# Kernel optimization log

Measured on AMD Instinct MI355X. Metric: run time of the kernel, lower is better.

## Reference

```python
import jax, jax.numpy as jnp
import numpy as np
from jax.ops import segment_sum

NEG_SLOPE = 0.01  # torch F.leaky_relu default

N_NODES = 100000
N_EDGES = 1600000
IN_FEAT = 67
HIDDEN = 256
N_CLASS = 18
N_GRAPHS = 256


def setup_inputs() -> dict:
    key = jax.random.key(0)
    ks = jax.random.split(key, 12)
    h = jax.random.normal(ks[0], (N_NODES, IN_FEAT), dtype=jnp.float32)
    src = jax.random.randint(ks[1], (N_EDGES,), 0, N_NODES, dtype=jnp.int32)
    dst = jax.random.randint(ks[2], (N_EDGES,), 0, N_NODES, dtype=jnp.int32)
    graph_ids = jnp.sort(jax.random.randint(ks[3], (N_NODES,), 0, N_GRAPHS, dtype=jnp.int32))
    s = 0.05
    W1_self = jax.random.normal(ks[4], (IN_FEAT, HIDDEN), dtype=jnp.float32) * s
    W1_neigh = jax.random.normal(ks[5], (IN_FEAT, HIDDEN), dtype=jnp.float32) * s
    b1 = jnp.zeros((HIDDEN,), dtype=jnp.float32)
    W2_self = jax.random.normal(ks[6], (HIDDEN, HIDDEN), dtype=jnp.float32) * s
    W2_neigh = jax.random.normal(ks[7], (HIDDEN, HIDDEN), dtype=jnp.float32) * s
    b2 = jnp.zeros((HIDDEN,), dtype=jnp.float32)
    Wfc = jax.random.normal(ks[8], (HIDDEN, N_CLASS), dtype=jnp.float32) * s
    bfc = jnp.zeros((N_CLASS,), dtype=jnp.float32)
    return {
        "h": h, "W1_self": W1_self, "W1_neigh": W1_neigh, "b1": b1,
        "W2_self": W2_self, "W2_neigh": W2_neigh, "b2": b2,
        "Wfc": Wfc, "bfc": bfc,
        "src": src, "dst": dst, "graph_ids": graph_ids, "num_graphs": N_GRAPHS,
    }


def _sage_mean(h, Wself, Wneigh, b, src, dst, n_nodes):
    # DGL SAGEConv(mean): h_neigh = mean over incoming neighbors; 0 if no neighbors
    agg = segment_sum(h[src], dst, num_segments=n_nodes)          # [N, D]
    deg = segment_sum(jnp.ones_like(dst, dtype=h.dtype), dst, num_segments=n_nodes)
    h_neigh = agg / jnp.maximum(deg, 1.0)[:, None]
    return h @ Wself + h_neigh @ Wneigh + b


def reference(h, W1_self, W1_neigh, b1, W2_self, W2_neigh, b2, Wfc, bfc,
              src, dst, graph_ids, num_graphs):
    n_nodes = h.shape[0]
    x = jax.nn.leaky_relu(_sage_mean(h, W1_self, W1_neigh, b1, src, dst, n_nodes), NEG_SLOPE)
    x = jax.nn.leaky_relu(_sage_mean(x, W2_self, W2_neigh, b2, src, dst, n_nodes), NEG_SLOPE)
    # dgl.mean_nodes: per-graph mean pooling over nodes
    gsum = segment_sum(x, graph_ids, num_segments=num_graphs)       # [G, D]
    gcnt = segment_sum(jnp.ones((n_nodes,), dtype=x.dtype), graph_ids, num_segments=num_graphs)
    hg = gsum / jnp.maximum(gcnt, 1.0)[:, None]
    return hg @ Wfc + bfc  # [G, n_classifier]
```

## Files before the change

kernel.cpp:

```cpp
#include <hip/hip_runtime.h>

#define WAVE 64
#define OW 256
#define LDA1 96
#define NCHUNK 64
#define PBITS 15
#define PBINS (1 << PBITS)
#define NPART 4

typedef short bf16x8 __attribute__((ext_vector_type(8)));
typedef float f32x4  __attribute__((ext_vector_type(4)));
typedef float f32x2  __attribute__((ext_vector_type(2)));

__device__ __forceinline__ unsigned short f2bf(float f) {
    unsigned int u = __float_as_uint(f);
    u = (u + 0x7FFF + ((u >> 16) & 1)) >> 16;
    return (unsigned short)u;
}
__device__ __forceinline__ float bf2f(unsigned short u) {
    return __uint_as_float(((unsigned int)u) << 16);
}
__device__ __forceinline__ float bflo(unsigned int u) { return __uint_as_float(u << 16); }
__device__ __forceinline__ float bfhi(unsigned int u) { return __uint_as_float(u & 0xFFFF0000u); }
__device__ __forceinline__ unsigned int packbf(float lo, float hi) {
    return (unsigned int)f2bf(lo) | ((unsigned int)f2bf(hi) << 16);
}
__device__ __forceinline__ float lrelu(float x) { return x > 0.0f ? x : 0.01f * x; }

__device__ __forceinline__ unsigned int pack4_f8(float v0, float v1, float v2, float v3) {
    int p = __builtin_amdgcn_cvt_pk_fp8_f32(v0, v1, 0, false);
    p = __builtin_amdgcn_cvt_pk_fp8_f32(v2, v3, p, true);
    return (unsigned int)p;
}
__device__ __forceinline__ unsigned char enc1_f8(float v) {
    return (unsigned char)(__builtin_amdgcn_cvt_pk_fp8_f32(v, 0.0f, 0, false) & 0xFF);
}
__device__ __forceinline__ void acc4_f8(float* a, unsigned int u) {
    f32x2 lo = __builtin_amdgcn_cvt_pk_f32_fp8(u, false);
    f32x2 hi = __builtin_amdgcn_cvt_pk_f32_fp8(u, true);
    a[0] += lo.x; a[1] += lo.y; a[2] += hi.x; a[3] += hi.y;
}


__device__ __forceinline__ void pack_b_body(const float* __restrict__ Ws,
                                            const float* __restrict__ Wn,
                                            unsigned short* __restrict__ Bb,
                                            int KHALF, int KT_HALF, int idx) {
    int e  = idx & 7;
    int l  = (idx >> 3) & 63;
    int nt = (idx >> 9) & 15;
    int kt = idx >> 13;
    int n  = nt * 16 + (l & 15);
    int kh = (kt < KT_HALF ? kt : kt - KT_HALF) * 32 + (l >> 4) * 8 + e;
    const float* W = (kt < KT_HALF) ? Ws : Wn;
    float v = (kh < KHALF) ? W[(size_t)kh * OW + n] : 0.0f;
    Bb[idx] = f2bf(v);
}

__global__ void prep_kernel(const float* __restrict__ h, unsigned int* __restrict__ hb,
                            unsigned int* __restrict__ hb8, int N, int K,
                            const float* __restrict__ W1s, const float* __restrict__ W1n,
                            unsigned short* __restrict__ Bb1,
                            const float* __restrict__ W2s, const float* __restrict__ W2n,
                            unsigned short* __restrict__ Bb2) {
    const int tid = blockIdx.x * blockDim.x + threadIdx.x;
    const int nth = gridDim.x * blockDim.x;

    const int tot_h = N * (LDA1 / 2);
    for (int i = tid; i < tot_h; i += nth) {
        int row = i / (LDA1 / 2);
        int c   = (i - row * (LDA1 / 2)) * 2;
        float v0 = (c     < K) ? h[(size_t)row * K + c]     : 0.0f;
        float v1 = (c + 1 < K) ? h[(size_t)row * K + c + 1] : 0.0f;
        hb[i] = packbf(v0, v1);
    }
    const int tot8 = N * (LDA1 / 4);
    for (int i = tid; i < tot8; i += nth) {
        int row = i / (LDA1 / 4);
        int c   = (i - row * (LDA1 / 4)) * 4;
        const float* hr = h + (size_t)row * K;
        float v0 = (c     < K) ? hr[c]     : 0.0f;
        float v1 = (c + 1 < K) ? hr[c + 1] : 0.0f;
        float v2 = (c + 2 < K) ? hr[c + 2] : 0.0f;
        float v3 = (c + 3 < K) ? hr[c + 3] : 0.0f;
        hb8[i] = pack4_f8(v0, v1, v2, v3);
    }
    for (int i = tid; i < 2 * 3 * 16 * 64 * 8; i += nth)
        pack_b_body(W1s, W1n, Bb1, K, 3, i);
    for (int i = tid; i < 2 * 8 * 16 * 64 * 8; i += nth)
        pack_b_body(W2s, W2n, Bb2, OW, 8, i);
}


__global__ __launch_bounds__(512) void hist_kernel(const int* __restrict__ dst, int E, int N,
                                                   unsigned short* __restrict__ hist,
                                                   unsigned short* __restrict__ rank_local) {
    __shared__ unsigned int lcnt[PBINS / 2];
    const int c    = blockIdx.x / NPART;
    const int p    = blockIdx.x - c * NPART;
    const int base = p << PBITS;
    const int nb   = (N - base < PBINS) ? (N - base) : PBINS;
    if (nb <= 0) return;
    const int che = (E + NCHUNK - 1) / NCHUNK;
    const int beg = c * che;
    const int end = (beg + che < E) ? (beg + che) : E;

    for (int i = threadIdx.x; i < PBINS / 2; i += 512) lcnt[i] = 0;
    __syncthreads();

    auto proc = [&](int d, int e) {
        d -= base;
        if ((unsigned)d < (unsigned)nb) {
            unsigned int sh  = (d & 1) * 16;
            unsigned int old = atomicAdd(&lcnt[d >> 1], 1u << sh);
            rank_local[e] = (unsigned short)((old >> sh) & 0xFFFFu);
        }
    };

    if (((beg | end) & 3) == 0) {
        const int4* dst4 = (const int4*)(dst + beg);
        const int n4 = (end - beg) >> 2;
        for (int i = threadIdx.x; i < n4; i += 512) {
            int4 d = dst4[i];
            int e = beg + 4 * i;
            proc(d.x, e + 0);
            proc(d.y, e + 1);
            proc(d.z, e + 2);
            proc(d.w, e + 3);
        }
    } else {
        for (int e = beg + (int)threadIdx.x; e < end; e += 512)
            proc(dst[e], e);
    }
    __syncthreads();

    unsigned short* hrow = hist + (size_t)c * N + base;
    for (int i = threadIdx.x; i < nb; i += 512) {
        unsigned int v = lcnt[i >> 1];
        hrow[i] = (unsigned short)((v >> ((i & 1) * 16)) & 0xFFFFu);
    }
}

__global__ void chunk_scan_kernel(unsigned short* __restrict__ hist, int* __restrict__ cnt,
                                  int N) {
    int bin = blockIdx.x * blockDim.x + threadIdx.x;
    if (bin >= N) return;
    int s = 0;
#pragma unroll 8
    for (int c = 0; c < NCHUNK; ++c) {
        size_t idx = (size_t)c * N + bin;
        int t = hist[idx];
        hist[idx] = (unsigned short)s;
        s += t;
    }
    cnt[bin] = s;
}

__global__ __launch_bounds__(1024) void scan_blocksum(const int* __restrict__ cnt,
                                                      int* __restrict__ bsum, int n) {
    __shared__ int s[1024];
    int i = blockIdx.x * 1024 + threadIdx.x;
    s[threadIdx.x] = (i < n) ? cnt[i] : 0;
    __syncthreads();
    for (int off = 512; off > 0; off >>= 1) {
        if (threadIdx.x < off) s[threadIdx.x] += s[threadIdx.x + off];
        __syncthreads();
    }
    if (threadIdx.x == 0) bsum[blockIdx.x] = s[0];
}

__global__ __launch_bounds__(128) void scan_offsets(int* __restrict__ bsum, int nb) {
    __shared__ int s[128];
    int v = (threadIdx.x < nb) ? bsum[threadIdx.x] : 0;
    s[threadIdx.x] = v;
    __syncthreads();
    for (int off = 1; off < 128; off <<= 1) {
        int t = (threadIdx.x >= off) ? s[threadIdx.x - off] : 0;
        __syncthreads();
        s[threadIdx.x] += t;
        __syncthreads();
    }
    if (threadIdx.x < nb) bsum[threadIdx.x] = s[threadIdx.x] - v;
}

__global__ __launch_bounds__(1024) void scan_write(const int* __restrict__ cnt,
                                                   const int* __restrict__ boff,
                                                   int* __restrict__ rowptr, int n) {
    __shared__ int s[1024];
    int i = blockIdx.x * 1024 + threadIdx.x;
    int v = (i < n) ? cnt[i] : 0;
    s[threadIdx.x] = v;
    __syncthreads();
    for (int off = 1; off < 1024; off <<= 1) {
        int t = (threadIdx.x >= off) ? s[threadIdx.x - off] : 0;
        __syncthreads();
        s[threadIdx.x] += t;
        __syncthreads();
    }
    if (i < n) rowptr[i + 1] = boff[blockIdx.x] + s[threadIdx.x];
    if (i == 0) rowptr[0] = 0;
}

__global__ void fill_kernel(const int* __restrict__ src, const int* __restrict__ dst,
                            const unsigned short* __restrict__ rank_local,
                            const int* __restrict__ rowptr,
                            const unsigned short* __restrict__ hist,
                            int* __restrict__ csr, int E, int N) {
    const int che = (E + NCHUNK - 1) / NCHUNK;
    const int tid = blockIdx.x * blockDim.x + threadIdx.x;
    const int nth = gridDim.x * blockDim.x;

    if ((che & 3) == 0) {
        const int e4 = E >> 2;
        const int4* dst4 = (const int4*)dst;
        const int4* src4 = (const int4*)src;
        const ushort4* r4 = (const ushort4*)rank_local;
        for (int i = tid; i < e4; i += nth) {
            int4 d = dst4[i];
            int4 s = src4[i];
            ushort4 r = r4[i];
            const unsigned short* hrow = hist + (size_t)(4 * i / che) * N;
            csr[rowptr[d.x] + (int)hrow[d.x] + (int)r.x] = s.x;
            csr[rowptr[d.y] + (int)hrow[d.y] + (int)r.y] = s.y;
            csr[rowptr[d.z] + (int)hrow[d.z] + (int)r.z] = s.z;
            csr[rowptr[d.w] + (int)hrow[d.w] + (int)r.w] = s.w;
        }
        for (int e = e4 * 4 + tid; e < E; e += nth) {
            int d = dst[e];
            csr[rowptr[d] + (int)hist[(size_t)(e / che) * N + d] + (int)rank_local[e]] = src[e];
        }
    } else {
        for (int e = tid; e < E; e += nth) {
            int d = dst[e];
            csr[rowptr[d] + (int)hist[(size_t)(e / che) * N + d] + (int)rank_local[e]] = src[e];
        }
    }
}


__global__ void gather_mean256_f8(const unsigned char* __restrict__ feat,
                                  const int* __restrict__ rowptr, const int* __restrict__ csr,
                                  unsigned int* __restrict__ aggm, int N) {
    const int lane = threadIdx.x & (WAVE - 1);
    const int grp  = lane >> 4;
    const int sub  = lane & 15;
    int wave = (blockIdx.x * blockDim.x + threadIdx.x) / WAVE;
    int nw   = (gridDim.x * blockDim.x) / WAVE;

    for (int v = wave; v < N; v += nw) {
        const int beg = rowptr[v], deg = rowptr[v + 1] - beg;
        float a[16];
#pragma unroll
        for (int i = 0; i < 16; ++i) a[i] = 0.0f;

        const int noct = deg >> 3;
        for (int i = 0; i < noct; ++i) {
            int e0 = csr[beg + 8 * i + grp];
            int e1 = csr[beg + 8 * i + 4 + grp];
            uint4 x0 = *(const uint4*)(feat + (size_t)e0 * 256 + sub * 16);
            uint4 x1 = *(const uint4*)(feat + (size_t)e1 * 256 + sub * 16);
            acc4_f8(a + 0,  x0.x); acc4_f8(a + 4,  x0.y);
            acc4_f8(a + 8,  x0.z); acc4_f8(a + 12, x0.w);
            acc4_f8(a + 0,  x1.x); acc4_f8(a + 4,  x1.y);
            acc4_f8(a + 8,  x1.z); acc4_f8(a + 12, x1.w);
        }
        for (int e = (noct << 3) + grp; e < deg; e += 4) {
            int s = csr[beg + e];
            uint4 x = *(const uint4*)(feat + (size_t)s * 256 + sub * 16);
            acc4_f8(a + 0,  x.x); acc4_f8(a + 4,  x.y);
            acc4_f8(a + 8,  x.z); acc4_f8(a + 12, x.w);
        }
#pragma unroll
        for (int i = 0; i < 16; ++i) {
            a[i] += __shfl_xor(a[i], 16);
            a[i] += __shfl_xor(a[i], 32);
        }
        if (grp == 0) {
            float inv = 1.0f / fmaxf((float)deg, 1.0f);
            unsigned int o[8];
#pragma unroll
            for (int i = 0; i < 8; ++i)
                o[i] = packbf(a[2 * i] * inv, a[2 * i + 1] * inv);
            unsigned int* dst0 = aggm + (size_t)v * 128 + sub * 8;
            *(uint4*)(dst0)     = make_uint4(o[0], o[1], o[2], o[3]);
            *(uint4*)(dst0 + 4) = make_uint4(o[4], o[5], o[6], o[7]);
        }
    }
}

__global__ void gather_mean_pad_f8(const unsigned char* __restrict__ feat,
                                   const int* __restrict__ rowptr, const int* __restrict__ csr,
                                   unsigned int* __restrict__ aggm, int N) {
    const int lane = threadIdx.x & (WAVE - 1);
    const int half = lane >> 5;
    const int sub  = lane & 31;
    const bool act = sub < 24;
    int wave = (blockIdx.x * blockDim.x + threadIdx.x) / WAVE;
    int nw   = (gridDim.x * blockDim.x) / WAVE;

    for (int v = wave; v < N; v += nw) {
        const int beg = rowptr[v], deg = rowptr[v + 1] - beg;
        const int npairs = deg >> 1;
        float a[4] = {0.f, 0.f, 0.f, 0.f};

        int p = 0;
        for (; p + 3 < npairs; p += 4) {
            int i0 = csr[beg + 2 * (p + 0) + half];
            int i1 = csr[beg + 2 * (p + 1) + half];
            int i2 = csr[beg + 2 * (p + 2) + half];
            int i3 = csr[beg + 2 * (p + 3) + half];
            if (act) {
                unsigned int x0 = *(const unsigned int*)(feat + (size_t)i0 * 96 + sub * 4);
                unsigned int x1 = *(const unsigned int*)(feat + (size_t)i1 * 96 + sub * 4);
                unsigned int x2 = *(const unsigned int*)(feat + (size_t)i2 * 96 + sub * 4);
                unsigned int x3 = *(const unsigned int*)(feat + (size_t)i3 * 96 + sub * 4);
                acc4_f8(a, x0); acc4_f8(a, x1); acc4_f8(a, x2); acc4_f8(a, x3);
            }
        }
        for (; p < npairs; ++p) {
            int i0 = csr[beg + 2 * p + half];
            if (act) {
                unsigned int x0 = *(const unsigned int*)(feat + (size_t)i0 * 96 + sub * 4);
                acc4_f8(a, x0);
            }
        }
        if ((deg & 1) && half == 0) {
            int i0 = csr[beg + deg - 1];
            if (act) {
                unsigned int x0 = *(const unsigned int*)(feat + (size_t)i0 * 96 + sub * 4);
                acc4_f8(a, x0);
            }
        }
#pragma unroll
        for (int i = 0; i < 4; ++i) a[i] += __shfl_xor(a[i], 32);

        if (half == 0 && act) {
            float inv = 1.0f / fmaxf((float)deg, 1.0f);
            uint2 o;
            o.x = packbf(a[0] * inv, a[1] * inv);
            o.y = packbf(a[2] * inv, a[3] * inv);
            *(uint2*)(aggm + (size_t)v * 48 + sub * 2) = o;
        }
    }
}

template<int KT_HALF, int CHUNK, bool F8OUT>
__global__ __launch_bounds__(256) void sage_mfma(
    const unsigned short* __restrict__ Hs, const unsigned short* __restrict__ Hn, int lda,
    const unsigned short* __restrict__ Bb, const float* __restrict__ bias,
    unsigned short* __restrict__ outb, unsigned char* __restrict__ out8, int M)
{
    constexpr int NT    = 2 * KT_HALF;
    constexpr int NCH   = NT / CHUNK;
    constexpr int CELEM = CHUNK * 16 * 64;
    constexpr int CPT   = CELEM / 256;
    __shared__ bf16x8 Bs[CELEM];

    const int t    = threadIdx.x;
    const int lane = t & 63, wid = t >> 6;
    const int wm   = wid >> 1, wn = wid & 1;
    const int brow = blockIdx.x * 64;
    const int lrow = lane & 15, kblk = lane >> 4;

    const int r0 = brow + wm * 32 + lrow;
    const int r1 = r0 + 16;
    const int r0c = (r0 < M) ? r0 : (M - 1);
    const int r1c = (r1 < M) ? r1 : (M - 1);

    f32x4 acc[2][8];
#pragma unroll
    for (int rt = 0; rt < 2; ++rt)
#pragma unroll
        for (int ct = 0; ct < 8; ++ct) acc[rt][ct] = (f32x4)0.0f;

    for (int ch = 0; ch < NCH; ++ch) {
        bf16x8 a0[CHUNK], a1[CHUNK];
#pragma unroll
        for (int k = 0; k < CHUNK; ++k) {
            int kt = ch * CHUNK + k;
            bool self = kt < KT_HALF;
            int kh = (self ? kt : kt - KT_HALF) * 32 + kblk * 8;
            const unsigned short* srcp = self ? Hs : Hn;
            a0[k] = *(const bf16x8*)(srcp + (size_t)r0c * lda + kh);
            a1[k] = *(const bf16x8*)(srcp + (size_t)r1c * lda + kh);
        }
        const bf16x8* gB = (const bf16x8*)Bb + (size_t)ch * CELEM;
        bf16x8 tmp[CPT];
#pragma unroll
        for (int i = 0; i < CPT; ++i) tmp[i] = gB[i * 256 + t];
        __syncthreads();
#pragma unroll
        for (int i = 0; i < CPT; ++i) Bs[i * 256 + t] = tmp[i];
        __syncthreads();
#pragma unroll
        for (int k = 0; k < CHUNK; ++k) {
            const bf16x8* bp = &Bs[(k * 16 + wn * 8) * 64 + lane];
#pragma unroll
            for (int ct = 0; ct < 8; ++ct) {
                bf16x8 b = bp[ct * 64];
                acc[0][ct] = __builtin_amdgcn_mfma_f32_16x16x32_bf16(a0[k], b, acc[0][ct], 0, 0, 0);
                acc[1][ct] = __builtin_amdgcn_mfma_f32_16x16x32_bf16(a1[k], b, acc[1][ct], 0, 0, 0);
            }
        }
    }

#pragma unroll
    for (int rt = 0; rt < 2; ++rt) {
        int rbase = brow + wm * 32 + rt * 16 + kblk * 4;
#pragma unroll
        for (int ct = 0; ct < 8; ++ct) {
            int col = wn * 128 + ct * 16 + lrow;
            float vb = bias[col];
#pragma unroll
            for (int j = 0; j < 4; ++j) {
                int row = rbase + j;
                if (row < M) {
                    float v = lrelu(acc[rt][ct][j] + vb);
                    outb[(size_t)row * OW + col] = f2bf(v);
                    if (F8OUT)
                        out8[(size_t)row * OW + col] = enc1_f8(v);
                }
            }
        }
    }
}


__global__ __launch_bounds__(256) void pool_fc_kernel(
    const unsigned short* __restrict__ x, const int* __restrict__ gid,
    const float* __restrict__ Wfc, const float* __restrict__ bfc,
    float* __restrict__ out, int N, int C)
{
    int g = blockIdx.x;
    int lo = 0, hi = N;
    while (lo < hi) { int m = (lo + hi) >> 1; if (gid[m] < g) lo = m + 1; else hi = m; }
    int beg = lo;
    hi = N;
    while (lo < hi) { int m = (lo + hi) >> 1; if (gid[m] <= g) lo = m + 1; else hi = m; }
    int end = lo;

    __shared__ float hg[OW];
    int c = threadIdx.x;
    float s0 = 0.f, s1 = 0.f, s2 = 0.f, s3 = 0.f;
    int r = beg;
    for (; r + 3 < end; r += 4) {
        s0 += bf2f(x[(size_t)(r + 0) * OW + c]);
        s1 += bf2f(x[(size_t)(r + 1) * OW + c]);
        s2 += bf2f(x[(size_t)(r + 2) * OW + c]);
        s3 += bf2f(x[(size_t)(r + 3) * OW + c]);
    }
    for (; r < end; ++r) s0 += bf2f(x[(size_t)r * OW + c]);
    float s = (s0 + s1) + (s2 + s3);
    float inv = (end > beg) ? 1.0f / (float)(end - beg) : 0.0f;
    hg[c] = s * inv;
    __syncthreads();

    if (c < C) {
        float a = bfc[c];
        for (int k = 0; k < OW; ++k)
            a = fmaf(hg[k], Wfc[(size_t)k * C + c], a);
        out[(size_t)g * C + c] = a;
    }
}

extern "C" void kernel_launch(void* const* d_in, const int* in_sizes, int n_in,
                              void* d_out, int out_size, void* d_ws, size_t ws_size,
                              hipStream_t stream) {
    const float* h   = (const float*)d_in[0];
    const float* W1s = (const float*)d_in[1];
    const float* W1n = (const float*)d_in[2];
    const float* b1  = (const float*)d_in[3];
    const float* W2s = (const float*)d_in[4];
    const float* W2n = (const float*)d_in[5];
    const float* b2  = (const float*)d_in[6];
    const float* Wfc = (const float*)d_in[7];
    const float* bfc = (const float*)d_in[8];
    const int*   src = (const int*)d_in[9];
    const int*   dst = (const int*)d_in[10];
    const int*   gid = (const int*)d_in[11];

    const int N  = in_sizes[11];
    const int E  = in_sizes[9];
    const int K1 = in_sizes[0] / N;
    const int NC = in_sizes[8];
    const int G  = out_size / NC;

    char* w = (char*)d_ws;
    auto alloc = [&](size_t bytes) { char* p = w; w += (bytes + 255) & ~(size_t)255; return p; };
    unsigned int*   hb     = (unsigned int*)alloc((size_t)N * (LDA1 / 2) * 4);
    unsigned int*   hb8    = (unsigned int*)alloc((size_t)N * LDA1);
    unsigned int*   agg1b  = (unsigned int*)alloc((size_t)N * (LDA1 / 2) * 4);
    unsigned short* x1b    = (unsigned short*)alloc((size_t)N * OW * 2);
    unsigned char*  x1f8   = (unsigned char*)alloc((size_t)N * OW);
    unsigned short* agg2b  = (unsigned short*)alloc((size_t)N * OW * 2);
    int*            rowptr = (int*)alloc((size_t)(N + 1) * 4);
    int*            cnt    = (int*)alloc((size_t)N * 4);
    int*            csr    = (int*)alloc((size_t)E * 4);
    unsigned short* rankl  = (unsigned short*)alloc((size_t)E * 2);
    unsigned short* hist   = (unsigned short*)alloc((size_t)NCHUNK * N * 2);
    int*            bsum   = (int*)alloc(1024 * 4);
    unsigned short* Bb1    = (unsigned short*)alloc((size_t)2 * 3 * 16 * 64 * 8 * 2);
    unsigned short* Bb2    = (unsigned short*)alloc((size_t)2 * 8 * 16 * 64 * 8 * 2);

    float* out = (float*)d_out;
    const int nb = (N + 1023) / 1024;

    hist_kernel<<<NCHUNK * NPART, 512, 0, stream>>>(dst, E, N, hist, rankl);
    chunk_scan_kernel<<<(N + 255) / 256, 256, 0, stream>>>(hist, cnt, N);
    scan_blocksum<<<nb, 1024, 0, stream>>>(cnt, bsum, N);
    scan_offsets<<<1, 128, 0, stream>>>(bsum, nb);
    scan_write<<<nb, 1024, 0, stream>>>(cnt, bsum, rowptr, N);
    fill_kernel<<<2048, 256, 0, stream>>>(src, dst, rankl, rowptr, hist, csr, E, N);

    prep_kernel<<<2048, 256, 0, stream>>>(h, hb, hb8, N, K1, W1s, W1n, Bb1, W2s, W2n, Bb2);

    const int gemm_grid = (N + 63) / 64;

    gather_mean_pad_f8<<<4096, 256, 0, stream>>>((const unsigned char*)hb8, rowptr, csr,
                                                 agg1b, N);
    sage_mfma<3, 2, true><<<gemm_grid, 256, 0, stream>>>((const unsigned short*)hb,
                                                         (const unsigned short*)agg1b, LDA1,
                                                         Bb1, b1, x1b, x1f8, N);

    gather_mean256_f8<<<4096, 256, 0, stream>>>(x1f8, rowptr, csr,
                                                (unsigned int*)agg2b, N);
    sage_mfma<8, 2, false><<<gemm_grid, 256, 0, stream>>>(x1b, agg2b, OW, Bb2, b2,
                                                          x1b, nullptr, N);

    pool_fc_kernel<<<G, 256, 0, stream>>>(x1b, gid, Wfc, bfc, out, N, NC);
}
```

Before: 357.9 us.

## Split 256-wide gather into column halves and enlarge GEMM row tile to 128

The second-layer neighbor gather now runs as two launches, each aggregating one 128-column half of the fp8 features, shrinking the per-pass working set to improve cache hit rates. The SAGE GEMM kernel now processes 128 rows per block (4 row tiles per wave), reusing each staged B chunk across more MFMAs. Costs are a second pass over the CSR indices and doubled accumulator registers, which may reduce occupancy.

```diff
diff --git a/kernel.cpp b/kernel.cpp
--- a/kernel.cpp
+++ b/kernel.cpp
@@ -240,50 +240,47 @@
 
 __global__ void gather_mean256_f8(const unsigned char* __restrict__ feat,
                                   const int* __restrict__ rowptr, const int* __restrict__ csr,
-                                  unsigned int* __restrict__ aggm, int N) {
+                                  unsigned int* __restrict__ aggm, int N, int colhalf) {
     const int lane = threadIdx.x & (WAVE - 1);
     const int grp  = lane >> 4;
     const int sub  = lane & 15;
+    const int cb   = colhalf * 128;
     int wave = (blockIdx.x * blockDim.x + threadIdx.x) / WAVE;
     int nw   = (gridDim.x * blockDim.x) / WAVE;
 
     for (int v = wave; v < N; v += nw) {
         const int beg = rowptr[v], deg = rowptr[v + 1] - beg;
-        float a[16];
-#pragma unroll
-        for (int i = 0; i < 16; ++i) a[i] = 0.0f;
+        float a[8];
+#pragma unroll
+        for (int i = 0; i < 8; ++i) a[i] = 0.0f;
 
         const int noct = deg >> 3;
         for (int i = 0; i < noct; ++i) {
             int e0 = csr[beg + 8 * i + grp];
             int e1 = csr[beg + 8 * i + 4 + grp];
-            uint4 x0 = *(const uint4*)(feat + (size_t)e0 * 256 + sub * 16);
-            uint4 x1 = *(const uint4*)(feat + (size_t)e1 * 256 + sub * 16);
-            acc4_f8(a + 0,  x0.x); acc4_f8(a + 4,  x0.y);
-            acc4_f8(a + 8,  x0.z); acc4_f8(a + 12, x0.w);
-            acc4_f8(a + 0,  x1.x); acc4_f8(a + 4,  x1.y);
-            acc4_f8(a + 8,  x1.z); acc4_f8(a + 12, x1.w);
+            uint2 x0 = *(const uint2*)(feat + (size_t)e0 * 256 + cb + sub * 8);
+            uint2 x1 = *(const uint2*)(feat + (size_t)e1 * 256 + cb + sub * 8);
+            acc4_f8(a + 0, x0.x); acc4_f8(a + 4, x0.y);
+            acc4_f8(a + 0, x1.x); acc4_f8(a + 4, x1.y);
         }
         for (int e = (noct << 3) + grp; e < deg; e += 4) {
             int s = csr[beg + e];
-            uint4 x = *(const uint4*)(feat + (size_t)s * 256 + sub * 16);
-            acc4_f8(a + 0,  x.x); acc4_f8(a + 4,  x.y);
-            acc4_f8(a + 8,  x.z); acc4_f8(a + 12, x.w);
-        }
-#pragma unroll
-        for (int i = 0; i < 16; ++i) {
+            uint2 x = *(const uint2*)(feat + (size_t)s * 256 + cb + sub * 8);
+            acc4_f8(a + 0, x.x); acc4_f8(a + 4, x.y);
+        }
+#pragma unroll
+        for (int i = 0; i < 8; ++i) {
             a[i] += __shfl_xor(a[i], 16);
             a[i] += __shfl_xor(a[i], 32);
         }
         if (grp == 0) {
             float inv = 1.0f / fmaxf((float)deg, 1.0f);
-            unsigned int o[8];
-#pragma unroll
-            for (int i = 0; i < 8; ++i)
-                o[i] = packbf(a[2 * i] * inv, a[2 * i + 1] * inv);
-            unsigned int* dst0 = aggm + (size_t)v * 128 + sub * 8;
-            *(uint4*)(dst0)     = make_uint4(o[0], o[1], o[2], o[3]);
-            *(uint4*)(dst0 + 4) = make_uint4(o[4], o[5], o[6], o[7]);
+            uint4 o;
+            o.x = packbf(a[0] * inv, a[1] * inv);
+            o.y = packbf(a[2] * inv, a[3] * inv);
+            o.z = packbf(a[4] * inv, a[5] * inv);
+            o.w = packbf(a[6] * inv, a[7] * inv);
+            *(uint4*)(aggm + (size_t)v * 128 + colhalf * 64 + sub * 4) = o;
         }
     }
 }
@@ -359,30 +356,33 @@
     const int t    = threadIdx.x;
     const int lane = t & 63, wid = t >> 6;
     const int wm   = wid >> 1, wn = wid & 1;
-    const int brow = blockIdx.x * 64;
+    const int brow = blockIdx.x * 128;
     const int lrow = lane & 15, kblk = lane >> 4;
 
-    const int r0 = brow + wm * 32 + lrow;
-    const int r1 = r0 + 16;
-    const int r0c = (r0 < M) ? r0 : (M - 1);
-    const int r1c = (r1 < M) ? r1 : (M - 1);
-
-    f32x4 acc[2][8];
-#pragma unroll
-    for (int rt = 0; rt < 2; ++rt)
+    int rc[4];
+#pragma unroll
+    for (int rt = 0; rt < 4; ++rt) {
+        int r = brow + wm * 64 + rt * 16 + lrow;
+        rc[rt] = (r < M) ? r : (M - 1);
+    }
+
+    f32x4 acc[4][8];
+#pragma unroll
+    for (int rt = 0; rt < 4; ++rt)
 #pragma unroll
         for (int ct = 0; ct < 8; ++ct) acc[rt][ct] = (f32x4)0.0f;
 
     for (int ch = 0; ch < NCH; ++ch) {
-        bf16x8 a0[CHUNK], a1[CHUNK];
+        bf16x8 a[CHUNK][4];
 #pragma unroll
         for (int k = 0; k < CHUNK; ++k) {
             int kt = ch * CHUNK + k;
             bool self = kt < KT_HALF;
             int kh = (self ? kt : kt - KT_HALF) * 32 + kblk * 8;
             const unsigned short* srcp = self ? Hs : Hn;
-            a0[k] = *(const bf16x8*)(srcp + (size_t)r0c * lda + kh);
-            a1[k] = *(const bf16x8*)(srcp + (size_t)r1c * lda + kh);
+#pragma unroll
+            for (int rt = 0; rt < 4; ++rt)
+                a[k][rt] = *(const bf16x8*)(srcp + (size_t)rc[rt] * lda + kh);
         }
         const bf16x8* gB = (const bf16x8*)Bb + (size_t)ch * CELEM;
         bf16x8 tmp[CPT];
@@ -398,15 +398,17 @@
 #pragma unroll
             for (int ct = 0; ct < 8; ++ct) {
                 bf16x8 b = bp[ct * 64];
-                acc[0][ct] = __builtin_amdgcn_mfma_f32_16x16x32_bf16(a0[k], b, acc[0][ct], 0, 0, 0);
-                acc[1][ct] = __builtin_amdgcn_mfma_f32_16x16x32_bf16(a1[k], b, acc[1][ct], 0, 0, 0);
+#pragma unroll
+                for (int rt = 0; rt < 4; ++rt)
+                    acc[rt][ct] = __builtin_amdgcn_mfma_f32_16x16x32_bf16(a[k][rt], b,
+                                                                          acc[rt][ct], 0, 0, 0);
             }
         }
     }
 
 #pragma unroll
-    for (int rt = 0; rt < 2; ++rt) {
-        int rbase = brow + wm * 32 + rt * 16 + kblk * 4;
+    for (int rt = 0; rt < 4; ++rt) {
+        int rbase = brow + wm * 64 + rt * 16 + kblk * 4;
 #pragma unroll
         for (int ct = 0; ct < 8; ++ct) {
             int col = wn * 128 + ct * 16 + lrow;
@@ -514,7 +516,7 @@
 
     prep_kernel<<<2048, 256, 0, stream>>>(h, hb, hb8, N, K1, W1s, W1n, Bb1, W2s, W2n, Bb2);
 
-    const int gemm_grid = (N + 63) / 64;
+    const int gemm_grid = (N + 127) / 128;
 
     gather_mean_pad_f8<<<4096, 256, 0, stream>>>((const unsigned char*)hb8, rowptr, csr,
                                                  agg1b, N);
@@ -523,7 +525,9 @@
                                                          Bb1, b1, x1b, x1f8, N);
 
     gather_mean256_f8<<<4096, 256, 0, stream>>>(x1f8, rowptr, csr,
-                                                (unsigned int*)agg2b, N);
+                                                (unsigned int*)agg2b, N, 0);
+    gather_mean256_f8<<<4096, 256, 0, stream>>>(x1f8, rowptr, csr,
+                                                (unsigned int*)agg2b, N, 1);
     sage_mfma<8, 2, false><<<gemm_grid, 256, 0, stream>>>(x1b, agg2b, OW, Bb2, b2,
                                                           x1b, nullptr, N);
 
```

Measured after the change: 440.6 us. 1.23x slower.
